# Kernel optimization log

Measured on AMD Instinct MI355X. Metric: run time of the kernel, lower is better.

Reference implementation:

```python
import jax, jax.numpy as jnp
import numpy as np

D_MODEL, D_STATE, D_CONV, EXPAND = 512, 16, 2, 2
D_INNER = EXPAND * D_MODEL          # 1024
DT_RANK = (D_MODEL + 15) // 16      # 32, mamba default ceil(d_model/16)
D_FF = 4 * D_MODEL                  # 2048
B, L = 8, 2048


def _mamba_params(key, prefix):
    ks = jax.random.split(key, 6)
    s = lambda k, shape, sc: (jax.random.normal(k, shape, jnp.float32) * sc)
    return {
        prefix + 'in_proj': s(ks[0], (2 * D_INNER, D_MODEL), 0.02),
        prefix + 'conv_w':  s(ks[1], (D_INNER, 1, D_CONV), 0.2),
        prefix + 'conv_b':  jnp.zeros((D_INNER,), jnp.float32),
        prefix + 'x_proj':  s(ks[2], (DT_RANK + 2 * D_STATE, D_INNER), 0.02),
        prefix + 'dt_w':    s(ks[3], (D_INNER, DT_RANK), 0.05),
        prefix + 'dt_b':    s(ks[4], (D_INNER,), 0.02) - 4.0,  # softplus -> small positive dt
        prefix + 'A_log':   jnp.log(jnp.broadcast_to(jnp.arange(1, D_STATE + 1, dtype=jnp.float32), (D_INNER, D_STATE))),
        prefix + 'Dskip':   jnp.ones((D_INNER,), jnp.float32),
        prefix + 'out_proj': s(ks[5], (D_MODEL, D_INNER), 0.02),
    }


def setup_inputs() -> dict:
    key = jax.random.key(0)
    kx, kf, kb, k1, k2, k3, k4 = jax.random.split(key, 7)
    inp = {'x': jax.random.normal(kx, (B, L, D_MODEL), jnp.float32)}
    inp.update(_mamba_params(kf, 'f_'))
    inp.update(_mamba_params(kb, 'b_'))
    inp.update({
        'ffn_w1': jax.random.normal(k1, (D_FF, D_MODEL), jnp.float32) * 0.02,
        'ffn_b1': jnp.zeros((D_FF,), jnp.float32),
        'ffn_w2': jax.random.normal(k2, (D_MODEL, D_FF), jnp.float32) * 0.02,
        'ffn_b2': jnp.zeros((D_MODEL,), jnp.float32),
        'ln1_g': jnp.ones((D_MODEL,), jnp.float32), 'ln1_b': jnp.zeros((D_MODEL,), jnp.float32),
        'ln2_g': jnp.ones((D_MODEL,), jnp.float32), 'ln2_b': jnp.zeros((D_MODEL,), jnp.float32),
    })
    return inp


def _mamba(x, in_proj, conv_w, conv_b, x_proj, dt_w, dt_b, A_log, Dskip, out_proj):
    """Standard Mamba block (selective SSM). x: (B, L, d_model) -> (B, L, d_model)."""
    Bb = x.shape[0]
    xz = jnp.einsum('bld,ed->ble', x, in_proj)         # (B, L, 2*d_inner)
    xi, z = jnp.split(xz, 2, axis=-1)
    # causal depthwise conv over time
    xc = jnp.transpose(xi, (0, 2, 1))                  # (B, d_inner, L)
    xc = jax.lax.conv_general_dilated(
        xc, conv_w, (1,), [(D_CONV - 1, 0)],
        dimension_numbers=('NCH', 'OIH', 'NCH'), feature_group_count=D_INNER)
    xi = jax.nn.silu(jnp.transpose(xc, (0, 2, 1)) + conv_b)  # (B, L, d_inner)
    # input-dependent dt, B, C
    x_dbl = jnp.einsum('bld,ed->ble', xi, x_proj)
    dt, Bm, Cm = jnp.split(x_dbl, [DT_RANK, DT_RANK + D_STATE], axis=-1)
    dt = jax.nn.softplus(jnp.einsum('blr,dr->bld', dt, dt_w) + dt_b)  # (B, L, d_inner)
    A = -jnp.exp(A_log)                                 # (d_inner, d_state)

    def step(h, inp):
        u_t, dt_t, B_t, C_t = inp                      # (B,d_inner),(B,d_inner),(B,d_state),(B,d_state)
        dA = jnp.exp(dt_t[..., None] * A)              # (B, d_inner, d_state)
        h = dA * h + (dt_t * u_t)[..., None] * B_t[:, None, :]
        y = jnp.einsum('bds,bs->bd', h, C_t)
        return h, y

    h0 = jnp.zeros((Bb, D_INNER, D_STATE), x.dtype)
    xs = (jnp.swapaxes(xi, 0, 1), jnp.swapaxes(dt, 0, 1),
          jnp.swapaxes(Bm, 0, 1), jnp.swapaxes(Cm, 0, 1))
    _, ys = jax.lax.scan(step, h0, xs)                 # ys: (L, B, d_inner)
    y = jnp.swapaxes(ys, 0, 1) + xi * Dskip
    y = y * jax.nn.silu(z)
    return jnp.einsum('bld,ed->ble', y, out_proj)


def _ln(x, g, b):
    m = x.mean(-1, keepdims=True)
    v = ((x - m) ** 2).mean(-1, keepdims=True)
    return (x - m) * jax.lax.rsqrt(v + 1e-5) * g + b


def reference(x,
              f_in_proj, f_conv_w, f_conv_b, f_x_proj, f_dt_w, f_dt_b, f_A_log, f_Dskip, f_out_proj,
              b_in_proj, b_conv_w, b_conv_b, b_x_proj, b_dt_w, b_dt_b, b_A_log, b_Dskip, b_out_proj,
              ffn_w1, ffn_b1, ffn_w2, ffn_b2, ln1_g, ln1_b, ln2_g, ln2_b):
    x_fwd = _mamba(x, f_in_proj, f_conv_w, f_conv_b, f_x_proj, f_dt_w, f_dt_b, f_A_log, f_Dskip, f_out_proj)
    x_bwd = jnp.flip(_mamba(jnp.flip(x, 1), b_in_proj, b_conv_w, b_conv_b, b_x_proj, b_dt_w, b_dt_b, b_A_log, b_Dskip, b_out_proj), 1)
    x = _ln(x + x_fwd + x_bwd, ln1_g, ln1_b)           # dropout = identity (eval)
    h = jax.nn.gelu(jnp.einsum('bld,fd->blf', x, ffn_w1) + ffn_b1, approximate=False)
    x_ffn = jnp.einsum('blf,df->bld', h, ffn_w2) + ffn_b2
    return _ln(x + x_ffn, ln2_g, ln2_b)
```

## Files before the change

kernel.cpp:

```cpp
#include <hip/hip_runtime.h>
#include <hip/hip_bf16.h>

#define BB 8
#define LL 2048
#define DM 512
#define DI 1024
#define DS 16
#define DTR 32
#define DFF 2048
#define BL (BB * LL)
#define CH 64
#define NCH (LL / CH)

typedef __hip_bfloat16 bf16;
struct bf4 { bf16 x, y, z, w; };
typedef __attribute__((ext_vector_type(8))) short short8;
typedef __attribute__((ext_vector_type(4))) float floatx4;

__device__ __forceinline__ float silu_f(float x) { return x / (1.f + __expf(-x)); }
__device__ __forceinline__ float softplus_f(float x) { return x > 20.f ? x : log1pf(__expf(x)); }
__device__ __forceinline__ float gelu_f(float x) { return 0.5f * x * (1.f + erff(x * 0.70710678118654752f)); }
__device__ __forceinline__ float b2f(bf16 v) { return __bfloat162float(v); }

__device__ __forceinline__ float4 ld4(const float* p) { return *(const float4*)p; }
__device__ __forceinline__ float4 ld4(const bf16* p) {
    bf4 v = *(const bf4*)p;
    return make_float4(b2f(v.x), b2f(v.y), b2f(v.z), b2f(v.w));
}
__device__ __forceinline__ bf4 pack4(float a, float b, float c, float d) {
    bf4 o; o.x = __float2bfloat16(a); o.y = __float2bfloat16(b);
    o.z = __float2bfloat16(c); o.w = __float2bfloat16(d); return o;
}

__device__ __forceinline__ void gll16(const bf16* g, bf16* l) {
    __builtin_amdgcn_global_load_lds(
        (const __attribute__((address_space(1))) void*)g,
        (__attribute__((address_space(3))) void*)l, 16, 0, 0);
}

enum { EP_BF16, EP_SOFTPLUS, EP_GELU, EP_F32, EP_RESF, EP_ACC, EP_BIASRES };

__global__ __launch_bounds__(256) void cvt_kernel(const float* __restrict__ in,
                                                  bf16* __restrict__ out, int n4)
{
    int i = blockIdx.x * 256 + threadIdx.x;
    if (i < n4) {
        float4 v = *(const float4*)(in + (size_t)i * 4);
        *(bf4*)(out + (size_t)i * 4) = pack4(v.x, v.y, v.z, v.w);
    }
}

template <int EPI, int BN>
__global__ __launch_bounds__(256) void gemm_mfma(
    const bf16* __restrict__ A, int lda,
    const bf16* __restrict__ W, int ldb,
    void* __restrict__ Cv, int ldc, int K,
    const float* __restrict__ bias, const void* __restrict__ resv)
{
    constexpr int BM = 128, BK = 64;
    constexpr int NT = BN / 32;
    constexpr int ACH_W = 4;
    constexpr int WCH_W = (BN / 8) / 4;
    constexpr int PITCH = BN + 8;
    constexpr int TILE_B = (BM + BN) * BK * 2;
    constexpr int STG_B = 32 * PITCH * 4;
    constexpr int SMEM_B = TILE_B > STG_B ? TILE_B : STG_B;
    __shared__ __align__(1024) char smem[SMEM_B];
    bf16* sA = (bf16*)smem;
    bf16* sW = (bf16*)(smem + BM * BK * 2);

    const int tid = threadIdx.x;
    const int wv = tid >> 6, ln = tid & 63;
    const int rch = ln >> 3;
    const int kgrp = (ln & 7) ^ (rch & 7);
    const int c = ln & 15, q4 = ln >> 4;
    const int m0 = blockIdx.x * BM, n0 = blockIdx.y * BN;
    const int wm = (wv >> 1) * 64, wn = (wv & 1) * (BN / 2);

    floatx4 acc[4][NT] = {};

    for (int k0 = 0; k0 < K; k0 += BK) {
        __syncthreads();
#pragma unroll
        for (int q = 0; q < ACH_W; ++q) {
            const int chunk = wv * ACH_W + q;
            gll16(A + (size_t)(m0 + chunk * 8 + rch) * lda + k0 + kgrp * 8,
                  sA + chunk * 512);
        }
#pragma unroll
        for (int q = 0; q < WCH_W; ++q) {
            const int chunk = wv * WCH_W + q;
            gll16(W + (size_t)(n0 + chunk * 8 + rch) * ldb + k0 + kgrp * 8,
                  sW + chunk * 512);
        }
        __syncthreads();

#pragma unroll
        for (int kk = 0; kk < 2; ++kk) {
            short8 af[4], wf[NT];
#pragma unroll
            for (int i = 0; i < 4; ++i)
                af[i] = *(const short8*)(sA + (wm + i * 16 + c) * 64 +
                                         (((kk << 2) | q4) ^ (c & 7)) * 8);
#pragma unroll
            for (int j = 0; j < NT; ++j)
                wf[j] = *(const short8*)(sW + (wn + j * 16 + c) * 64 +
                                         (((kk << 2) | q4) ^ (c & 7)) * 8);
#pragma unroll
            for (int i = 0; i < 4; ++i)
#pragma unroll
                for (int j = 0; j < NT; ++j)
                    acc[i][j] = __builtin_amdgcn_mfma_f32_16x16x32_bf16(
                        af[i], wf[j], acc[i][j], 0, 0, 0);
        }
    }

    constexpr int ELEMS = (32 * BN) / 256;
    constexpr int TPR = BN / ELEMS;
    float* sC = (float*)smem;
    const int row_l = tid / TPR;
    const int cg = (tid % TPR) * ELEMS;
    const int mg = m0 + (row_l & 15) + ((row_l >> 4) * 64);

#pragma unroll
    for (int i = 0; i < 4; ++i) {
        __syncthreads();
#pragma unroll
        for (int j = 0; j < NT; ++j)
#pragma unroll
            for (int r = 0; r < 4; ++r)
                sC[((wv >> 1) * 16 + q4 * 4 + r) * PITCH + wn + j * 16 + c] = acc[i][j][r];
        __syncthreads();

        const int m = mg + i * 16;
        const int nb = n0 + cg;
        const size_t co = (size_t)m * ldc + nb;
        float v[ELEMS];
#pragma unroll
        for (int e = 0; e < ELEMS; ++e) v[e] = sC[row_l * PITCH + cg + e];

        if constexpr (EPI == EP_BF16 || EPI == EP_GELU) {
            bf16 ov[ELEMS];
#pragma unroll
            for (int e = 0; e < ELEMS; ++e) {
                float t = v[e];
                if constexpr (EPI == EP_GELU) t = gelu_f(t + bias[nb + e]);
                ov[e] = __float2bfloat16(t);
            }
#pragma unroll
            for (int q = 0; q < ELEMS / 8; ++q)
                *(uint4*)((bf16*)Cv + co + q * 8) = *(const uint4*)(ov + q * 8);
        } else {
#pragma unroll
            for (int e = 0; e < ELEMS; ++e) {
                if constexpr (EPI == EP_RESF)
                    v[e] += ((const float*)resv)[co + e];
                else if constexpr (EPI == EP_ACC)
                    v[e] += ((const float*)Cv)[co + e];
                else if constexpr (EPI == EP_BIASRES)
                    v[e] += bias[nb + e] + b2f(((const bf16*)resv)[co + e]);
            }
#pragma unroll
            for (int q = 0; q < ELEMS / 4; ++q) {
                float4 o = {v[q * 4 + 0], v[q * 4 + 1], v[q * 4 + 2], v[q * 4 + 3]};
                *(float4*)((float*)Cv + co + q * 4) = o;
            }
        }
    }
}

template <int EPI, typename TA>
__global__ __launch_bounds__(256) void gemm_nt(
    const TA* __restrict__ A, int lda,
    const float* __restrict__ W, int ldb,
    void* __restrict__ Cv, int ldc,
    int K,
    const float* __restrict__ bias,
    const void* __restrict__ resv)
{
    __shared__ float As[16][64];
    __shared__ float Bs[16][64];
    const int tid = threadIdx.x;
    const int tx = tid & 15, ty = tid >> 4;
    const int m0 = blockIdx.y * 64, n0 = blockIdx.x * 64;
    const int lrow = tid >> 2;
    const int lcol = (tid & 3) << 2;

    const TA* Ap = A + (size_t)(m0 + lrow) * lda + lcol;
    const float* Bp = W + (size_t)(n0 + lrow) * ldb + lcol;

    float acc[4][4] = {};

    for (int k0 = 0; k0 < K; k0 += 16) {
        float4 av = ld4(Ap + k0);
        float4 bv = ld4(Bp + k0);
        __syncthreads();
        As[lcol + 0][lrow] = av.x; As[lcol + 1][lrow] = av.y;
        As[lcol + 2][lrow] = av.z; As[lcol + 3][lrow] = av.w;
        Bs[lcol + 0][lrow] = bv.x; Bs[lcol + 1][lrow] = bv.y;
        Bs[lcol + 2][lrow] = bv.z; Bs[lcol + 3][lrow] = bv.w;
        __syncthreads();
#pragma unroll
        for (int kk = 0; kk < 16; ++kk) {
            float4 a4 = *(const float4*)(&As[kk][ty << 2]);
            float4 b4 = *(const float4*)(&Bs[kk][tx << 2]);
            float aa[4] = {a4.x, a4.y, a4.z, a4.w};
            float bb[4] = {b4.x, b4.y, b4.z, b4.w};
#pragma unroll
            for (int i = 0; i < 4; ++i)
#pragma unroll
                for (int j = 0; j < 4; ++j)
                    acc[i][j] = fmaf(aa[i], bb[j], acc[i][j]);
        }
    }

#pragma unroll
    for (int i = 0; i < 4; ++i) {
        const int m = m0 + (ty << 2) + i;
        const int n = n0 + (tx << 2);
        float v[4] = {acc[i][0], acc[i][1], acc[i][2], acc[i][3]};
        const size_t co = (size_t)m * ldc + n;
        if constexpr (EPI == EP_SOFTPLUS) {
            *(bf4*)((bf16*)Cv + co) = pack4(
                softplus_f(v[0] + bias[n + 0]), softplus_f(v[1] + bias[n + 1]),
                softplus_f(v[2] + bias[n + 2]), softplus_f(v[3] + bias[n + 3]));
        } else if constexpr (EPI == EP_F32) {
            float4 o = {v[0], v[1], v[2], v[3]};
            *(float4*)((float*)Cv + co) = o;
        }
    }
}

__global__ __launch_bounds__(256) void conv_silu_kernel(
    const bf16* __restrict__ xz, const float* __restrict__ cw,
    const float* __restrict__ cb, bf16* __restrict__ xic, int nbr)
{
    const int idx = blockIdx.x * 256 + threadIdx.x;
    const int c4 = (idx & 255) << 2;
    const int row = idx >> 8;
    const int l = row & (LL - 1);
    const int lnbr = l + nbr;
    const bool valid = (lnbr >= 0) && (lnbr < LL);

    const bf16* pc = xz + (size_t)row * (2 * DI) + c4;
    float4 cur = ld4(pc);
    float4 prv = make_float4(0.f, 0.f, 0.f, 0.f);
    if (valid) prv = ld4(pc + (ptrdiff_t)nbr * (2 * DI));

    float w0[4], w1[4];
#pragma unroll
    for (int q = 0; q < 4; ++q) { w0[q] = cw[(c4 + q) * 2]; w1[q] = cw[(c4 + q) * 2 + 1]; }
    float4 bb = ld4(cb + c4);

    *(bf4*)(xic + (size_t)row * DI + c4) = pack4(
        silu_f(fmaf(w0[0], prv.x, fmaf(w1[0], cur.x, bb.x))),
        silu_f(fmaf(w0[1], prv.y, fmaf(w1[1], cur.y, bb.y))),
        silu_f(fmaf(w0[2], prv.z, fmaf(w1[2], cur.z, bb.z))),
        silu_f(fmaf(w0[3], prv.w, fmaf(w1[3], cur.w, bb.w))));
}

__global__ __launch_bounds__(256) void scan_p1(
    const bf16* __restrict__ xic, const bf16* __restrict__ dtb,
    const float* __restrict__ xdb, const float* __restrict__ A_log,
    float* __restrict__ SD, float* __restrict__ H, int t0, int tstep)
{
    const int g = blockIdx.x * 256 + threadIdx.x;
    const int d = g & (DI - 1);
    const int rest = g >> 10;
    const int chunk = rest & (NCH - 1);
    const int b = rest >> 5;

    float a[DS], h[DS];
    bool fast = true;
#pragma unroll
    for (int s = 0; s < DS; ++s) {
        a[s] = -__expf(A_log[d * DS + s]);
        h[s] = 0.f;
        fast = fast && (fabsf(a[s] + (float)(s + 1)) < 1e-3f * (s + 1));
    }

    __shared__ float sB[CH][DS];
    for (int i = threadIdx.x; i < CH * DS; i += 256) {
        const int it = i >> 4, s = i & 15;
        const int t = t0 + (chunk * CH + it) * tstep;
        sB[it][s] = xdb[((size_t)(b * LL + t)) * 64 + DTR + s];
    }
    __syncthreads();

    float sumdt = 0.f;
    if (fast) {
        for (int it = 0; it < CH; ++it) {
            const int t = t0 + (chunk * CH + it) * tstep;
            const size_t row = (size_t)(b * LL + t);
            const float dtv = b2f(dtb[row * DI + d]);
            const float u = b2f(xic[row * DI + d]);
            sumdt += dtv;
            const float du = dtv * u;
            const float e = __expf(-dtv);
            float dA = 1.f;
#pragma unroll
            for (int s = 0; s < DS; ++s) {
                dA *= e;
                h[s] = fmaf(dA, h[s], du * sB[it][s]);
            }
        }
    } else {
        for (int it = 0; it < CH; ++it) {
            const int t = t0 + (chunk * CH + it) * tstep;
            const size_t row = (size_t)(b * LL + t);
            const float dtv = b2f(dtb[row * DI + d]);
            const float u = b2f(xic[row * DI + d]);
            sumdt += dtv;
            const float du = dtv * u;
#pragma unroll
            for (int s = 0; s < DS; ++s)
                h[s] = fmaf(__expf(dtv * a[s]), h[s], du * sB[it][s]);
        }
    }
    SD[((size_t)(b * NCH + chunk)) * DI + d] = sumdt;
    const size_t base = ((size_t)((b * NCH + chunk) * DS)) * DI + d;
#pragma unroll
    for (int s = 0; s < DS; ++s)
        H[base + (size_t)s * DI] = h[s];
}

__global__ __launch_bounds__(256) void scan_p2(
    const float* __restrict__ SD, float* __restrict__ H,
    const float* __restrict__ A_log)
{
    const int g = blockIdx.x * 256 + threadIdx.x;
    const int d = g & (DI - 1);
    const int rest = g >> 10;
    const int s = rest & 15;
    const int b = rest >> 4;
    const float a = -__expf(A_log[d * DS + s]);
    float h = 0.f;
    for (int c = 0; c < NCH; ++c) {
        const float sd = SD[((size_t)(b * NCH + c)) * DI + d];
        const size_t idx = ((size_t)((b * NCH + c) * DS + s)) * DI + d;
        const float Pv = __expf(a * sd);
        const float Hv = H[idx];
        H[idx] = h;
        h = fmaf(Pv, h, Hv);
    }
}

__global__ __launch_bounds__(256) void scan_p3(
    const bf16* __restrict__ xic, const bf16* __restrict__ xz,
    const float* __restrict__ xdb, bf16* __restrict__ dty,
    const float* __restrict__ A_log, const float* __restrict__ Dskip,
    const float* __restrict__ H, int t0, int tstep)
{
    const int g = blockIdx.x * 256 + threadIdx.x;
    const int d = g & (DI - 1);
    const int rest = g >> 10;
    const int chunk = rest & (NCH - 1);
    const int b = rest >> 5;

    float a[DS], h[DS];
    bool fast = true;
    const size_t base = ((size_t)((b * NCH + chunk) * DS)) * DI + d;
#pragma unroll
    for (int s = 0; s < DS; ++s) {
        a[s] = -__expf(A_log[d * DS + s]);
        h[s] = H[base + (size_t)s * DI];
        fast = fast && (fabsf(a[s] + (float)(s + 1)) < 1e-3f * (s + 1));
    }
    const float dsk = Dskip[d];

    __shared__ float sBC[CH][2 * DS];
    for (int i = threadIdx.x; i < CH * 2 * DS; i += 256) {
        const int it = i >> 5, j = i & 31;
        const int t = t0 + (chunk * CH + it) * tstep;
        sBC[it][j] = xdb[((size_t)(b * LL + t)) * 64 + DTR + j];
    }
    __syncthreads();

    if (fast) {
        for (int it = 0; it < CH; ++it) {
            const int t = t0 + (chunk * CH + it) * tstep;
            const size_t row = (size_t)(b * LL + t);
            const float dtv = b2f(dty[row * DI + d]);
            const float u = b2f(xic[row * DI + d]);
            const float zv = b2f(xz[row * (2 * DI) + DI + d]);
            const float du = dtv * u;
            const float e = __expf(-dtv);
            float dA = 1.f, y = 0.f;
#pragma unroll
            for (int s = 0; s < DS; ++s) {
                dA *= e;
                h[s] = fmaf(dA, h[s], du * sBC[it][s]);
                y = fmaf(h[s], sBC[it][DS + s], y);
            }
            y = fmaf(u, dsk, y);
            dty[row * DI + d] = __float2bfloat16(y * silu_f(zv));
        }
    } else {
        for (int it = 0; it < CH; ++it) {
            const int t = t0 + (chunk * CH + it) * tstep;
            const size_t row = (size_t)(b * LL + t);
            const float dtv = b2f(dty[row * DI + d]);
            const float u = b2f(xic[row * DI + d]);
            const float zv = b2f(xz[row * (2 * DI) + DI + d]);
            const float du = dtv * u;
            float y = 0.f;
#pragma unroll
            for (int s = 0; s < DS; ++s) {
                h[s] = fmaf(__expf(dtv * a[s]), h[s], du * sBC[it][s]);
                y = fmaf(h[s], sBC[it][DS + s], y);
            }
            y = fmaf(u, dsk, y);
            dty[row * DI + d] = __float2bfloat16(y * silu_f(zv));
        }
    }
}

template <int OUTF>
__global__ __launch_bounds__(256) void ln_kernel(
    const float* __restrict__ in, const float* __restrict__ g,
    const float* __restrict__ bta, void* __restrict__ outv)
{
    const int row = blockIdx.x;
    const int t = threadIdx.x;
    const float* p = in + (size_t)row * DM;
    const float v0 = p[t];
    const float v1 = p[t + 256];
    float sm = v0 + v1;
    float sq = v0 * v0 + v1 * v1;
#pragma unroll
    for (int off = 32; off > 0; off >>= 1) {
        sm += __shfl_xor(sm, off);
        sq += __shfl_xor(sq, off);
    }
    __shared__ float red[8];
    const int w = t >> 6;
    if ((t & 63) == 0) { red[w] = sm; red[4 + w] = sq; }
    __syncthreads();
    sm = red[0] + red[1] + red[2] + red[3];
    sq = red[4] + red[5] + red[6] + red[7];
    const float mean = sm * (1.f / DM);
    const float var = sq * (1.f / DM) - mean * mean;
    const float rstd = rsqrtf(var + 1e-5f);
    const float o0 = (v0 - mean) * rstd * g[t] + bta[t];
    const float o1 = (v1 - mean) * rstd * g[t + 256] + bta[t + 256];
    if constexpr (OUTF == 0) {
        bf16* out = (bf16*)outv;
        out[(size_t)row * DM + t] = __float2bfloat16(o0);
        out[(size_t)row * DM + t + 256] = __float2bfloat16(o1);
    } else {
        float* out = (float*)outv;
        out[(size_t)row * DM + t] = o0;
        out[(size_t)row * DM + t + 256] = o1;
    }
}

extern "C" void kernel_launch(void* const* d_in, const int* in_sizes, int n_in,
                              void* d_out, int out_size, void* d_ws, size_t ws_size,
                              hipStream_t stream)
{
    const float* x = (const float*)d_in[0];
    const float* ffn_w1 = (const float*)d_in[19];
    const float* ffn_b1 = (const float*)d_in[20];
    const float* ffn_w2 = (const float*)d_in[21];
    const float* ffn_b2 = (const float*)d_in[22];
    const float* ln1_g = (const float*)d_in[23];
    const float* ln1_b = (const float*)d_in[24];
    const float* ln2_g = (const float*)d_in[25];
    const float* ln2_b = (const float*)d_in[26];

    char* p = (char*)d_ws;
    auto alloc = [&](size_t bytes) { void* r = (void*)p; p += (bytes + 255) & ~(size_t)255; return r; };
    bf16* xz   = (bf16*)alloc((size_t)BL * 2048 * 2);
    bf16* xic  = (bf16*)alloc((size_t)BL * DI * 2);
    bf16* dtb  = (bf16*)alloc((size_t)BL * DI * 2);
    float* xdb = (float*)alloc((size_t)BL * 64 * 4);
    float* sum = (float*)alloc((size_t)BL * DM * 4);
    bf16* x1   = (bf16*)alloc((size_t)BL * DM * 2);
    bf16* xb   = (bf16*)alloc((size_t)BL * DM * 2);
    float* SD  = (float*)alloc((size_t)BB * NCH * DI * 4);
    float* Hc  = (float*)alloc((size_t)BB * NCH * DS * DI * 4);
    bf16* wip[2], *wxp[2], *wop[2];
    for (int d = 0; d < 2; ++d) {
        wip[d] = (bf16*)alloc((size_t)2 * DI * DM * 2);
        wxp[d] = (bf16*)alloc((size_t)64 * DI * 2);
        wop[d] = (bf16*)alloc((size_t)DM * DI * 2);
    }
    bf16* w1b = (bf16*)alloc((size_t)DFF * DM * 2);
    bf16* w2b = (bf16*)alloc((size_t)DM * DFF * 2);

    auto cvt = [&](const float* src, bf16* dst, size_t n) {
        int n4 = (int)(n / 4);
        cvt_kernel<<<(n4 + 255) / 256, 256, 0, stream>>>(src, dst, n4);
    };
    cvt(x, xb, (size_t)BL * DM);
    for (int d = 0; d < 2; ++d) {
        const int o = 1 + d * 9;
        cvt((const float*)d_in[o + 0], wip[d], (size_t)2 * DI * DM);
        cvt((const float*)d_in[o + 3], wxp[d], (size_t)64 * DI);
        cvt((const float*)d_in[o + 8], wop[d], (size_t)DM * DI);
    }
    cvt(ffn_w1, w1b, (size_t)DFF * DM);
    cvt(ffn_w2, w2b, (size_t)DM * DFF);

    const dim3 blk(256);
    for (int dir = 0; dir < 2; ++dir) {
        const int o = 1 + dir * 9;
        const float* conv_w = (const float*)d_in[o + 1];
        const float* conv_b = (const float*)d_in[o + 2];
        const float* dt_w   = (const float*)d_in[o + 4];
        const float* dt_b   = (const float*)d_in[o + 5];
        const float* A_log  = (const float*)d_in[o + 6];
        const float* Dskip  = (const float*)d_in[o + 7];

        const int nbr = (dir == 0) ? -1 : +1;
        const int t0 = (dir == 0) ? 0 : (LL - 1);
        const int tstep = (dir == 0) ? 1 : -1;

        gemm_mfma<EP_BF16, 128><<<dim3(BL / 128, (2 * DI) / 128), blk, 0, stream>>>(
            xb, DM, wip[dir], DM, xz, 2 * DI, DM, nullptr, nullptr);
        conv_silu_kernel<<<BL, blk, 0, stream>>>(xz, conv_w, conv_b, xic, nbr);
        gemm_mfma<EP_F32, 64><<<dim3(BL / 128, 1), blk, 0, stream>>>(
            xic, DI, wxp[dir], DI, xdb, 64, DI, nullptr, nullptr);
        gemm_nt<EP_SOFTPLUS, float><<<dim3(DI / 64, BL / 64), blk, 0, stream>>>(
            xdb, 64, dt_w, DTR, dtb, DI, DTR, dt_b, nullptr);

        scan_p1<<<(BB * NCH * DI) / 256, blk, 0, stream>>>(
            xic, dtb, xdb, A_log, SD, Hc, t0, tstep);
        scan_p2<<<(BB * DS * DI) / 256, blk, 0, stream>>>(SD, Hc, A_log);
        scan_p3<<<(BB * NCH * DI) / 256, blk, 0, stream>>>(
            xic, xz, xdb, dtb, A_log, Dskip, Hc, t0, tstep);

        if (dir == 0)
            gemm_mfma<EP_RESF, 128><<<dim3(BL / 128, DM / 128), blk, 0, stream>>>(
                dtb, DI, wop[dir], DI, sum, DM, DI, nullptr, x);
        else
            gemm_mfma<EP_ACC, 128><<<dim3(BL / 128, DM / 128), blk, 0, stream>>>(
                dtb, DI, wop[dir], DI, sum, DM, DI, nullptr, nullptr);
    }

    ln_kernel<0><<<BL, blk, 0, stream>>>(sum, ln1_g, ln1_b, x1);
    gemm_mfma<EP_GELU, 128><<<dim3(BL / 128, DFF / 128), blk, 0, stream>>>(
        x1, DM, w1b, DM, xz, DFF, DM, ffn_b1, nullptr);
    gemm_mfma<EP_BIASRES, 128><<<dim3(BL / 128, DM / 128), blk, 0, stream>>>(
        xz, DFF, w2b, DFF, sum, DM, DFF, ffn_b2, x1);
    ln_kernel<1><<<BL, blk, 0, stream>>>(sum, ln2_g, ln2_b, d_out);
}
```

Baseline: 863.2 us.

## Merge both out_proj GEMMs into one K=2048 GEMM and shrink GEMM BK

The two directional out_proj GEMMs become a single GEMM. The scan outputs of both directions go into one interleaved 2048-wide buffer, and a concatenated, packed out_proj weight is built. This removes one launch and the read-modify-write of the fp32 sum buffer done by the EP_ACC epilogue. Separately, the MFMA GEMM K-tile drops from 64 to 32 with a new LDS swizzle, which halves shared memory per block and may raise occupancy. The cost is twice as many barrier iterations per K, and the strided 2048-pitch dt/y accesses in the scan kernels.

```diff
diff --git a/kernel.cpp b/kernel.cpp
--- a/kernel.cpp
+++ b/kernel.cpp
@@ -11,6 +11,7 @@
 #define BL (BB * LL)
 #define CH 64
 #define NCH (LL / CH)
+#define YL 2048
 
 typedef __hip_bfloat16 bf16;
 struct bf4 { bf16 x, y, z, w; };
@@ -38,7 +39,7 @@
         (__attribute__((address_space(3))) void*)l, 16, 0, 0);
 }
 
-enum { EP_BF16, EP_SOFTPLUS, EP_GELU, EP_F32, EP_RESF, EP_ACC, EP_BIASRES };
+enum { EP_BF16, EP_SOFTPLUS, EP_GELU, EP_F32, EP_RESF, EP_BIASRES };
 
 __global__ __launch_bounds__(256) void cvt_kernel(const float* __restrict__ in,
                                                   bf16* __restrict__ out, int n4)
@@ -47,6 +48,22 @@
     if (i < n4) {
         float4 v = *(const float4*)(in + (size_t)i * 4);
         *(bf4*)(out + (size_t)i * 4) = pack4(v.x, v.y, v.z, v.w);
+    }
+}
+
+__global__ __launch_bounds__(256) void cvt_pack_kernel(
+    const float* __restrict__ wf, const float* __restrict__ wb,
+    bf16* __restrict__ out, int n4)
+{
+    int i = blockIdx.x * 256 + threadIdx.x;
+    if (i < n4) {
+        const int pos = i * 4;
+        const int n = pos >> 11;
+        const int c = pos & 2047;
+        const float* src = (c < 1024) ? (wf + (size_t)n * 1024 + c)
+                                      : (wb + (size_t)n * 1024 + (c - 1024));
+        float4 v = *(const float4*)src;
+        *(bf4*)(out + (size_t)pos) = pack4(v.x, v.y, v.z, v.w);
     }
 }
 
@@ -57,23 +74,24 @@
     void* __restrict__ Cv, int ldc, int K,
     const float* __restrict__ bias, const void* __restrict__ resv)
 {
-    constexpr int BM = 128, BK = 64;
+    constexpr int BM = 128, BK = 32;
     constexpr int NT = BN / 32;
-    constexpr int ACH_W = 4;
-    constexpr int WCH_W = (BN / 8) / 4;
+    constexpr int ACH_W = 2;
+    constexpr int WCH_W = (BN / 16) / 4;
     constexpr int PITCH = BN + 8;
-    constexpr int TILE_B = (BM + BN) * BK * 2;
+    constexpr int TILE_B = BM * 64 + BN * 64;
     constexpr int STG_B = 32 * PITCH * 4;
     constexpr int SMEM_B = TILE_B > STG_B ? TILE_B : STG_B;
     __shared__ __align__(1024) char smem[SMEM_B];
     bf16* sA = (bf16*)smem;
-    bf16* sW = (bf16*)(smem + BM * BK * 2);
+    bf16* sW = (bf16*)(smem + BM * 64);
 
     const int tid = threadIdx.x;
     const int wv = tid >> 6, ln = tid & 63;
-    const int rch = ln >> 3;
-    const int kgrp = (ln & 7) ^ (rch & 7);
+    const int rloc = ln >> 2;
+    const int kperm = (ln & 3) ^ ((ln >> 3) & 3);
     const int c = ln & 15, q4 = ln >> 4;
+    const int swz8 = 8 * (q4 ^ ((c >> 1) & 3));
     const int m0 = blockIdx.x * BM, n0 = blockIdx.y * BN;
     const int wm = (wv >> 1) * 64, wn = (wv & 1) * (BN / 2);
 
@@ -84,35 +102,30 @@
 #pragma unroll
         for (int q = 0; q < ACH_W; ++q) {
             const int chunk = wv * ACH_W + q;
-            gll16(A + (size_t)(m0 + chunk * 8 + rch) * lda + k0 + kgrp * 8,
+            gll16(A + (size_t)(m0 + chunk * 16 + rloc) * lda + k0 + kperm * 8,
                   sA + chunk * 512);
         }
 #pragma unroll
         for (int q = 0; q < WCH_W; ++q) {
             const int chunk = wv * WCH_W + q;
-            gll16(W + (size_t)(n0 + chunk * 8 + rch) * ldb + k0 + kgrp * 8,
+            gll16(W + (size_t)(n0 + chunk * 16 + rloc) * ldb + k0 + kperm * 8,
                   sW + chunk * 512);
         }
         __syncthreads();
 
-#pragma unroll
-        for (int kk = 0; kk < 2; ++kk) {
-            short8 af[4], wf[NT];
-#pragma unroll
-            for (int i = 0; i < 4; ++i)
-                af[i] = *(const short8*)(sA + (wm + i * 16 + c) * 64 +
-                                         (((kk << 2) | q4) ^ (c & 7)) * 8);
+        short8 af[4], wf[NT];
+#pragma unroll
+        for (int i = 0; i < 4; ++i)
+            af[i] = *(const short8*)(sA + (wm + i * 16 + c) * 32 + swz8);
+#pragma unroll
+        for (int j = 0; j < NT; ++j)
+            wf[j] = *(const short8*)(sW + (wn + j * 16 + c) * 32 + swz8);
+#pragma unroll
+        for (int i = 0; i < 4; ++i)
 #pragma unroll
             for (int j = 0; j < NT; ++j)
-                wf[j] = *(const short8*)(sW + (wn + j * 16 + c) * 64 +
-                                         (((kk << 2) | q4) ^ (c & 7)) * 8);
-#pragma unroll
-            for (int i = 0; i < 4; ++i)
-#pragma unroll
-                for (int j = 0; j < NT; ++j)
-                    acc[i][j] = __builtin_amdgcn_mfma_f32_16x16x32_bf16(
-                        af[i], wf[j], acc[i][j], 0, 0, 0);
-        }
+                acc[i][j] = __builtin_amdgcn_mfma_f32_16x16x32_bf16(
+                    af[i], wf[j], acc[i][j], 0, 0, 0);
     }
 
     constexpr int ELEMS = (32 * BN) / 256;
@@ -155,8 +168,6 @@
             for (int e = 0; e < ELEMS; ++e) {
                 if constexpr (EPI == EP_RESF)
                     v[e] += ((const float*)resv)[co + e];
-                else if constexpr (EPI == EP_ACC)
-                    v[e] += ((const float*)Cv)[co + e];
                 else if constexpr (EPI == EP_BIASRES)
                     v[e] += bias[nb + e] + b2f(((const bf16*)resv)[co + e]);
             }
@@ -260,7 +271,7 @@
 }
 
 __global__ __launch_bounds__(256) void scan_p1(
-    const bf16* __restrict__ xic, const bf16* __restrict__ dtb,
+    const bf16* __restrict__ xic, const bf16* __restrict__ ydt,
     const float* __restrict__ xdb, const float* __restrict__ A_log,
     float* __restrict__ SD, float* __restrict__ H, int t0, int tstep)
 {
@@ -292,7 +303,7 @@
         for (int it = 0; it < CH; ++it) {
             const int t = t0 + (chunk * CH + it) * tstep;
             const size_t row = (size_t)(b * LL + t);
-            const float dtv = b2f(dtb[row * DI + d]);
+            const float dtv = b2f(ydt[row * YL + d]);
             const float u = b2f(xic[row * DI + d]);
             sumdt += dtv;
             const float du = dtv * u;
@@ -308,7 +319,7 @@
         for (int it = 0; it < CH; ++it) {
             const int t = t0 + (chunk * CH + it) * tstep;
             const size_t row = (size_t)(b * LL + t);
-            const float dtv = b2f(dtb[row * DI + d]);
+            const float dtv = b2f(ydt[row * YL + d]);
             const float u = b2f(xic[row * DI + d]);
             sumdt += dtv;
             const float du = dtv * u;
@@ -380,7 +391,7 @@
         for (int it = 0; it < CH; ++it) {
             const int t = t0 + (chunk * CH + it) * tstep;
             const size_t row = (size_t)(b * LL + t);
-            const float dtv = b2f(dty[row * DI + d]);
+            const float dtv = b2f(dty[row * YL + d]);
             const float u = b2f(xic[row * DI + d]);
             const float zv = b2f(xz[row * (2 * DI) + DI + d]);
             const float du = dtv * u;
@@ -393,13 +404,13 @@
                 y = fmaf(h[s], sBC[it][DS + s], y);
             }
             y = fmaf(u, dsk, y);
-            dty[row * DI + d] = __float2bfloat16(y * silu_f(zv));
+            dty[row * YL + d] = __float2bfloat16(y * silu_f(zv));
         }
     } else {
         for (int it = 0; it < CH; ++it) {
             const int t = t0 + (chunk * CH + it) * tstep;
             const size_t row = (size_t)(b * LL + t);
-            const float dtv = b2f(dty[row * DI + d]);
+            const float dtv = b2f(dty[row * YL + d]);
             const float u = b2f(xic[row * DI + d]);
             const float zv = b2f(xz[row * (2 * DI) + DI + d]);
             const float du = dtv * u;
@@ -410,7 +421,7 @@
                 y = fmaf(h[s], sBC[it][DS + s], y);
             }
             y = fmaf(u, dsk, y);
-            dty[row * DI + d] = __float2bfloat16(y * silu_f(zv));
+            dty[row * YL + d] = __float2bfloat16(y * silu_f(zv));
         }
     }
 }
@@ -470,21 +481,21 @@
 
     char* p = (char*)d_ws;
     auto alloc = [&](size_t bytes) { void* r = (void*)p; p += (bytes + 255) & ~(size_t)255; return r; };
-    bf16* xz   = (bf16*)alloc((size_t)BL * 2048 * 2);
-    bf16* xic  = (bf16*)alloc((size_t)BL * DI * 2);
-    bf16* dtb  = (bf16*)alloc((size_t)BL * DI * 2);
-    float* xdb = (float*)alloc((size_t)BL * 64 * 4);
-    float* sum = (float*)alloc((size_t)BL * DM * 4);
-    bf16* x1   = (bf16*)alloc((size_t)BL * DM * 2);
-    bf16* xb   = (bf16*)alloc((size_t)BL * DM * 2);
-    float* SD  = (float*)alloc((size_t)BB * NCH * DI * 4);
-    float* Hc  = (float*)alloc((size_t)BB * NCH * DS * DI * 4);
-    bf16* wip[2], *wxp[2], *wop[2];
+    bf16* xz    = (bf16*)alloc((size_t)BL * 2048 * 2);
+    bf16* xic   = (bf16*)alloc((size_t)BL * DI * 2);
+    bf16* ybuf  = (bf16*)alloc((size_t)BL * YL * 2);
+    float* xdb  = (float*)alloc((size_t)BL * 64 * 4);
+    float* sum  = (float*)alloc((size_t)BL * DM * 4);
+    bf16* x1    = (bf16*)alloc((size_t)BL * DM * 2);
+    bf16* xb    = (bf16*)alloc((size_t)BL * DM * 2);
+    float* SD   = (float*)alloc((size_t)BB * NCH * DI * 4);
+    float* Hc   = (float*)alloc((size_t)BB * NCH * DS * DI * 4);
+    bf16* wip[2], *wxp[2];
     for (int d = 0; d < 2; ++d) {
         wip[d] = (bf16*)alloc((size_t)2 * DI * DM * 2);
         wxp[d] = (bf16*)alloc((size_t)64 * DI * 2);
-        wop[d] = (bf16*)alloc((size_t)DM * DI * 2);
-    }
+    }
+    bf16* wopcat = (bf16*)alloc((size_t)DM * YL * 2);
     bf16* w1b = (bf16*)alloc((size_t)DFF * DM * 2);
     bf16* w2b = (bf16*)alloc((size_t)DM * DFF * 2);
 
@@ -497,8 +508,9 @@
         const int o = 1 + d * 9;
         cvt((const float*)d_in[o + 0], wip[d], (size_t)2 * DI * DM);
         cvt((const float*)d_in[o + 3], wxp[d], (size_t)64 * DI);
-        cvt((const float*)d_in[o + 8], wop[d], (size_t)DM * DI);
-    }
+    }
+    cvt_pack_kernel<<<(DM * YL / 4 + 255) / 256, 256, 0, stream>>>(
+        (const float*)d_in[9], (const float*)d_in[18], wopcat, DM * YL / 4);
     cvt(ffn_w1, w1b, (size_t)DFF * DM);
     cvt(ffn_w2, w2b, (size_t)DM * DFF);
 
@@ -515,6 +527,7 @@
         const int nbr = (dir == 0) ? -1 : +1;
         const int t0 = (dir == 0) ? 0 : (LL - 1);
         const int tstep = (dir == 0) ? 1 : -1;
+        bf16* ydt = ybuf + (size_t)dir * 1024;
 
         gemm_mfma<EP_BF16, 128><<<dim3(BL / 128, (2 * DI) / 128), blk, 0, stream>>>(
             xb, DM, wip[dir], DM, xz, 2 * DI, DM, nullptr, nullptr);
@@ -522,21 +535,17 @@
         gemm_mfma<EP_F32, 64><<<dim3(BL / 128, 1), blk, 0, stream>>>(
             xic, DI, wxp[dir], DI, xdb, 64, DI, nullptr, nullptr);
         gemm_nt<EP_SOFTPLUS, float><<<dim3(DI / 64, BL / 64), blk, 0, stream>>>(
-            xdb, 64, dt_w, DTR, dtb, DI, DTR, dt_b, nullptr);
+            xdb, 64, dt_w, DTR, ydt, YL, DTR, dt_b, nullptr);
 
         scan_p1<<<(BB * NCH * DI) / 256, blk, 0, stream>>>(
-            xic, dtb, xdb, A_log, SD, Hc, t0, tstep);
+            xic, ydt, xdb, A_log, SD, Hc, t0, tstep);
         scan_p2<<<(BB * DS * DI) / 256, blk, 0, stream>>>(SD, Hc, A_log);
         scan_p3<<<(BB * NCH * DI) / 256, blk, 0, stream>>>(
-            xic, xz, xdb, dtb, A_log, Dskip, Hc, t0, tstep);
-
-        if (dir == 0)
-            gemm_mfma<EP_RESF, 128><<<dim3(BL / 128, DM / 128), blk, 0, stream>>>(
-                dtb, DI, wop[dir], DI, sum, DM, DI, nullptr, x);
-        else
-            gemm_mfma<EP_ACC, 128><<<dim3(BL / 128, DM / 128), blk, 0, stream>>>(
-                dtb, DI, wop[dir], DI, sum, DM, DI, nullptr, nullptr);
-    }
+            xic, xz, xdb, ydt, A_log, Dskip, Hc, t0, tstep);
+    }
+
+    gemm_mfma<EP_RESF, 128><<<dim3(BL / 128, DM / 128), blk, 0, stream>>>(
+        ybuf, YL, wopcat, YL, sum, DM, YL, nullptr, x);
 
     ln_kernel<0><<<BL, blk, 0, stream>>>(sum, ln1_g, ln1_b, x1);
     gemm_mfma<EP_GELU, 128><<<dim3(BL / 128, DFF / 128), blk, 0, stream>>>(
```

After: 885.3 us. 2.6% more time.
